# Kernel optimization log

Hardware: AMD Instinct MI355X
Metric: run time of the kernel (lower is better)

The kernel has to match this reference:

```python
import jax, jax.numpy as jnp
import numpy as np

N = 50000
E = 800000
IN_C, HID, OUT_C, HEADS = 128, 32, 64, 4
NEG_SLOPE = 0.2


def setup_inputs() -> dict:
    key = jax.random.key(0)
    ks = jax.random.split(key, 10)
    x = jax.random.normal(ks[0], (N, IN_C), dtype=jnp.float32)
    edge_index = jax.random.randint(ks[1], (2, E), 0, N, dtype=jnp.int64)
    s = 0.05
    W1 = jax.random.normal(ks[2], (IN_C, HID), dtype=jnp.float32) * s
    b1 = jnp.zeros((HID,), dtype=jnp.float32)
    Wg = jax.random.normal(ks[3], (HID, HEADS * HID), dtype=jnp.float32) * s
    ag_src = jax.random.normal(ks[4], (HEADS, HID), dtype=jnp.float32) * s
    ag_dst = jax.random.normal(ks[5], (HEADS, HID), dtype=jnp.float32) * s
    bg = jnp.zeros((HID,), dtype=jnp.float32)
    W2 = jax.random.normal(ks[6], (HID, OUT_C), dtype=jnp.float32) * s
    b2 = jnp.zeros((OUT_C,), dtype=jnp.float32)
    return {"x": x, "edge_index": edge_index, "W1": W1, "b1": b1,
            "Wg": Wg, "ag_src": ag_src, "ag_dst": ag_dst, "bg": bg,
            "W2": W2, "b2": b2}


def _add_self_loops(edge_index, n):
    loop = jnp.arange(n, dtype=edge_index.dtype)
    return jnp.concatenate([edge_index, jnp.stack([loop, loop])], axis=1)


def _gcn(x, src, dst, W, b, n):
    # PyG GCNConv: symmetric normalization with self-loops, scatter-add
    xw = x @ W  # [N, F]
    deg = jnp.zeros((n,), xw.dtype).at[dst].add(1.0)  # in-degree incl self-loops
    dinv = jax.lax.rsqrt(deg)
    norm = dinv[src] * dinv[dst]  # [E']
    msg = xw[src] * norm[:, None]  # [E', F]
    out = jax.ops.segment_sum(msg, dst, num_segments=n)
    return out + b


def _gat(x, src, dst, Wg, a_src, a_dst, b, n):
    # PyG GATConv, concat=False (mean over heads), leaky_relu slope 0.2
    h = (x @ Wg).reshape(n, HEADS, HID)  # [N, H, D]
    al_s = jnp.einsum('nhd,hd->nh', h, a_src)  # [N, H]
    al_d = jnp.einsum('nhd,hd->nh', h, a_dst)
    logits = jax.nn.leaky_relu(al_s[src] + al_d[dst], NEG_SLOPE)  # [E', H]
    # segment softmax over incoming edges of each dst node
    m = jax.ops.segment_max(logits, dst, num_segments=n)
    e = jnp.exp(logits - m[dst])
    denom = jax.ops.segment_sum(e, dst, num_segments=n)
    alpha = e / denom[dst]  # [E', H]
    msg = h[src] * alpha[:, :, None]  # [E', H, D]
    out = jax.ops.segment_sum(msg, dst, num_segments=n)  # [N, H, D]
    return out.mean(axis=1) + b


def reference(x, edge_index, W1, b1, Wg, ag_src, ag_dst, bg, W2, b2):
    ei = _add_self_loops(edge_index, N)
    src, dst = ei[0], ei[1]
    h = jax.nn.relu(_gcn(x, src, dst, W1, b1, N))
    h = jax.nn.relu(_gat(h, src, dst, Wg, ag_src, ag_dst, bg, N))
    return _gcn(h, src, dst, W2, b2, N)
```

## Files before the change

### kernel.cpp

```cpp
#include <hip/hip_runtime.h>
#include <hip/hip_bf16.h>

#define N_NODES 50000
#define N_EDGES 800000
#define EP (N_EDGES + N_NODES)
#define IN_C 128
#define HID 32
#define OUT_C 64
#define HEADS 4
#define NEG_SLOPE 0.2f

#define NPB 128
#define K_BUCKETS ((N_NODES + NPB - 1) / NPB)

typedef unsigned int uint32;

__device__ __forceinline__ float bf_lo(uint32 u) { return __uint_as_float(u << 16); }
__device__ __forceinline__ float bf_hi(uint32 u) { return __uint_as_float(u & 0xffff0000u); }
__device__ __forceinline__ uint32 f2bf(float f) {
    uint32 u = __float_as_uint(f);
    return (u + 0x7fffu + ((u >> 16) & 1u)) >> 16;
}
__device__ __forceinline__ uint32 pack_bf2(float a, float b) {
    return f2bf(a) | (f2bf(b) << 16);
}

__global__ __launch_bounds__(512) void k_init2(int* __restrict__ gcnt,
                                               const float* __restrict__ Wg,
                                               const float* __restrict__ ags,
                                               const float* __restrict__ agd,
                                               float* __restrict__ wals,
                                               float* __restrict__ wald,
                                               const float* __restrict__ W2,
                                               uint32* __restrict__ wgp,
                                               uint32* __restrict__ w2p) {
    int t = threadIdx.x;
    if (t < K_BUCKETS + 1) gcnt[t] = 0;
    if (t < 256) {
        int c = t & 127;
        int h = c >> 5, k = c & 31;
        const float* a = (t < 128) ? ags : agd;
        float acc = 0.f;
#pragma unroll
        for (int d = 0; d < 32; d++) acc += Wg[k * 128 + h * 32 + d] * a[h * 32 + d];
        if (t < 128) wals[c] = acc; else wald[c] = acc;
    }
    for (int i = t; i < 2048; i += 512) {
        int j4 = i >> 6, d = (i >> 1) & 31, pp = i & 1;
        int c0 = 4 * j4 + 2 * pp, c1 = c0 + 1;
        float a = Wg[(c0 & 31) * 128 + (c0 >> 5) * 32 + d];
        float b = Wg[(c1 & 31) * 128 + (c1 >> 5) * 32 + d];
        wgp[i] = pack_bf2(a, b);
    }
    for (int i = t; i < 1024; i += 512) {
        int k4 = i >> 7, d = (i >> 1) & 63, pp = i & 1;
        int r0 = 4 * k4 + 2 * pp, r1 = r0 + 1;
        w2p[i] = pack_bf2(W2[r0 * 64 + d], W2[r1 * 64 + d]);
    }
}


__global__ __launch_bounds__(256) void k_bcount(const int* __restrict__ ei,
                                                int* __restrict__ gcnt) {
    __shared__ int h[K_BUCKETS];
    int t = threadIdx.x;
    for (int i = t; i < K_BUCKETS; i += 256) h[i] = 0;
    __syncthreads();
    int base = blockIdx.x * 4096;
    int dd[16];
#pragma unroll
    for (int k = 0; k < 16; k++) {
        int e = base + k * 256 + t;
        dd[k] = (e < N_EDGES) ? ei[N_EDGES + e] : -1;
    }
#pragma unroll
    for (int k = 0; k < 16; k++)
        if (dd[k] >= 0) atomicAdd(&h[dd[k] >> 7], 1);
    __syncthreads();
    for (int i = t; i < K_BUCKETS; i += 256)
        if (h[i]) atomicAdd(&gcnt[i], h[i]);
}

__global__ __launch_bounds__(512) void k_bscan(const int* __restrict__ gcnt,
                                               int* __restrict__ gbase,
                                               int* __restrict__ gcursor) {
    __shared__ int sd[512];
    int t = threadIdx.x;
    int v = (t < K_BUCKETS) ? gcnt[t] : 0;
    sd[t] = v;
    __syncthreads();
    for (int off = 1; off < 512; off <<= 1) {
        int x = (t >= off) ? sd[t - off] : 0;
        __syncthreads();
        sd[t] += x;
        __syncthreads();
    }
    if (t < K_BUCKETS) {
        int excl = sd[t] - v;
        gbase[t] = excl;
        gcursor[t] = excl;
    }
    if (t == 0) gbase[K_BUCKETS] = sd[K_BUCKETS - 1];
}

__global__ __launch_bounds__(256) void k_bucket(const int* __restrict__ ei,
                                                int* __restrict__ gcursor,
                                                uint32* __restrict__ gpairs) {
    __shared__ int cnt[K_BUCKETS];
    __shared__ int bas[K_BUCKETS];
    int t = threadIdx.x;
    for (int i = t; i < K_BUCKETS; i += 256) cnt[i] = 0;
    __syncthreads();
    int base = blockIdx.x * 2048;
    int ss[8], dd[8], ml[8];
#pragma unroll
    for (int k = 0; k < 8; k++) {
        int e = base + k * 256 + t;
        ss[k] = (e < N_EDGES) ? ei[e] : -1;
        dd[k] = (e < N_EDGES) ? ei[N_EDGES + e] : 0;
    }
#pragma unroll
    for (int k = 0; k < 8; k++)
        if (ss[k] >= 0) ml[k] = atomicAdd(&cnt[dd[k] >> 7], 1);
    __syncthreads();
    for (int i = t; i < K_BUCKETS; i += 256)
        bas[i] = cnt[i] ? atomicAdd(&gcursor[i], cnt[i]) : 0;
    __syncthreads();
#pragma unroll
    for (int k = 0; k < 8; k++)
        if (ss[k] >= 0)
            gpairs[bas[dd[k] >> 7] + ml[k]] = ((uint32)ss[k] << 7) | (uint32)(dd[k] & 127);
}

__global__ __launch_bounds__(256) void k_node(const uint32* __restrict__ gpairs,
                                              const int* __restrict__ gbase,
                                              int* __restrict__ offs,
                                              float* __restrict__ dinv,
                                              int* __restrict__ srcs) {
    __shared__ int cnt[NPB];
    __shared__ int scn[NPB];
    __shared__ int cur[NPB];
    int t = threadIdx.x;
    int b = blockIdx.x;
    int lo = b << 7;
    int nn = N_NODES - lo; if (nn > NPB) nn = NPB;
    int pb = gbase[b], pe = gbase[b + 1];
    if (t < NPB) cnt[t] = 0;
    __syncthreads();
    for (int i = pb + t; i < pe; i += 256)
        atomicAdd(&cnt[gpairs[i] & 127], 1);
    __syncthreads();
    if (t < NPB) scn[t] = cnt[t];
    __syncthreads();
    for (int off = 1; off < NPB; off <<= 1) {
        int x = 0;
        if (t >= off && t < NPB) x = scn[t - off];
        __syncthreads();
        if (t < NPB) scn[t] += x;
        __syncthreads();
    }
    if (t < nn) {
        int excl = scn[t] - cnt[t];
        int o = pb + excl + lo + t;
        offs[lo + t] = o;
        cur[t] = o;
        dinv[lo + t] = rsqrtf((float)(cnt[t] + 1));
        srcs[pb + scn[t] + lo + t] = lo + t;
    }
    if (b == K_BUCKETS - 1 && t == 0) offs[N_NODES] = pe + N_NODES;
    __syncthreads();
    for (int i = pb + t; i < pe; i += 256) {
        uint32 u = gpairs[i];
        int pos = atomicAdd(&cur[u & 127], 1);
        srcs[pos] = (int)(u >> 7);
    }
}

__global__ __launch_bounds__(256) void k_gemm1(const float* __restrict__ x,
                                               const float* __restrict__ W1,
                                               const float* __restrict__ dinv,
                                               uint32* __restrict__ xw1) {
    __shared__ float wl[IN_C * HID];
    __shared__ float xl[8 * IN_C];
    int t = threadIdx.x;
    for (int i = t; i < IN_C * HID; i += 256) {
        int k = i >> 5, f = i & 31;
        wl[(k >> 1) * 64 + f * 2 + (k & 1)] = W1[i];
    }
    int nb = blockIdx.x * 8;
    const float4* x4 = (const float4*)(x + (size_t)nb * IN_C);
    ((float4*)xl)[t] = x4[t];
    __syncthreads();
    int g = t >> 5, f = t & 31;
    const float2* xr = (const float2*)(xl + g * IN_C);
    const float2* wp = (const float2*)wl;
    float acc = 0.f;
#pragma unroll 16
    for (int k2 = 0; k2 < 64; k2++) {
        float2 xv = xr[k2];
        float2 wv = wp[k2 * 32 + f];
        acc += xv.x * wv.x + xv.y * wv.y;
    }
    float v = acc * dinv[nb + g];
    float vn = __shfl_xor(v, 1, 64);
    if ((f & 1) == 0) xw1[(size_t)(nb + g) * 16 + (f >> 1)] = pack_bf2(v, vn);
}

__global__ __launch_bounds__(256) void k_gather1(const uint32* __restrict__ xw1,
                                                 const int* __restrict__ offs,
                                                 const int* __restrict__ srcs,
                                                 const float* __restrict__ dinv,
                                                 const float* __restrict__ b1,
                                                 const float* __restrict__ wals,
                                                 const float* __restrict__ wald,
                                                 uint32* __restrict__ h1s,
                                                 float* __restrict__ als,
                                                 float* __restrict__ ald) {
    int t = threadIdx.x;
    int l16 = t & 15;
    int n = blockIdx.x * 16 + (t >> 4);
    int s0 = offs[n], s1 = offs[n + 1];
    const uint32* xc = xw1 + l16;
    float a0 = 0.f, a1 = 0.f, a2 = 0.f, a3 = 0.f;
    int j = s0;
    for (; j + 1 < s1; j += 2) {
        uint32 uA = xc[(size_t)srcs[j] * 16];
        uint32 uB = xc[(size_t)srcs[j + 1] * 16];
        a0 += bf_lo(uA); a1 += bf_hi(uA);
        a2 += bf_lo(uB); a3 += bf_hi(uB);
    }
    if (j < s1) {
        uint32 uA = xc[(size_t)srcs[j] * 16];
        a0 += bf_lo(uA); a1 += bf_hi(uA);
    }
    float dn = dinv[n];
    float2 b = ((const float2*)b1)[l16];
    float vx = (a0 + a2) * dn + b.x;
    float vy = (a1 + a3) * dn + b.y;
    vx = vx > 0.f ? vx : 0.f;
    vy = vy > 0.f ? vy : 0.f;
    h1s[(size_t)n * 16 + l16] = pack_bf2(vx, vy);

    float ps0, ps1, ps2, ps3, pd0, pd1, pd2, pd3;
    {
        float2 w0 = ((const float2*)wals)[0 * 16 + l16];
        float2 w1 = ((const float2*)wals)[1 * 16 + l16];
        float2 w2 = ((const float2*)wals)[2 * 16 + l16];
        float2 w3 = ((const float2*)wals)[3 * 16 + l16];
        ps0 = vx * w0.x + vy * w0.y;
        ps1 = vx * w1.x + vy * w1.y;
        ps2 = vx * w2.x + vy * w2.y;
        ps3 = vx * w3.x + vy * w3.y;
        float2 u0 = ((const float2*)wald)[0 * 16 + l16];
        float2 u1 = ((const float2*)wald)[1 * 16 + l16];
        float2 u2 = ((const float2*)wald)[2 * 16 + l16];
        float2 u3 = ((const float2*)wald)[3 * 16 + l16];
        pd0 = vx * u0.x + vy * u0.y;
        pd1 = vx * u1.x + vy * u1.y;
        pd2 = vx * u2.x + vy * u2.y;
        pd3 = vx * u3.x + vy * u3.y;
    }
#pragma unroll
    for (int m = 1; m < 16; m <<= 1) {
        ps0 += __shfl_xor(ps0, m, 16); ps1 += __shfl_xor(ps1, m, 16);
        ps2 += __shfl_xor(ps2, m, 16); ps3 += __shfl_xor(ps3, m, 16);
        pd0 += __shfl_xor(pd0, m, 16); pd1 += __shfl_xor(pd1, m, 16);
        pd2 += __shfl_xor(pd2, m, 16); pd3 += __shfl_xor(pd3, m, 16);
    }
    if (l16 == 0) {
        als[n * 4 + 0] = ps0; als[n * 4 + 1] = ps1;
        als[n * 4 + 2] = ps2; als[n * 4 + 3] = ps3;
        ald[n * 4 + 0] = pd0; ald[n * 4 + 1] = pd1;
        ald[n * 4 + 2] = pd2; ald[n * 4 + 3] = pd3;
    }
}

__global__ __launch_bounds__(256) void k_gat_agg(const uint32* __restrict__ h1s,
                                                 const float* __restrict__ als,
                                                 const float* __restrict__ ald,
                                                 const int* __restrict__ offs,
                                                 const int* __restrict__ srcs,
                                                 const uint32* __restrict__ wgp,
                                                 const float* __restrict__ bg,
                                                 const float* __restrict__ dinv,
                                                 uint32* __restrict__ h2s) {
    __shared__ __align__(16) uint32 wl[2048];
    __shared__ __align__(16) uint32 gl[8][64];
    int t = threadIdx.x;
    {
        const uint4* src4 = (const uint4*)wgp;
        uint4* dst4 = (uint4*)wl;
        dst4[t] = src4[t];
        dst4[256 + t] = src4[256 + t];
    }

    int l32 = t & 31;
    int hb = t & 32;
    int g8 = t >> 5;
    int n = blockIdx.x * 8 + g8;
    int h = l32 >> 3, e8 = l32 & 7;
    int l16 = l32 & 15;
    int h16 = (l32 >> 4) & 1;
    int s0 = offs[n], s1 = offs[n + 1];
    float ad = ald[n * 4 + h];
    const uint32* rowp = h1s + l16;

    float g00 = 0.f, g01 = 0.f, g10 = 0.f, g11 = 0.f;
    float g20 = 0.f, g21 = 0.f, g30 = 0.f, g31 = 0.f;
    float ssum = 0.f;
    for (int base = s0; base < s1; base += 8) {
        int jj = base + e8;
        int sA = 0; float wt = 0.f;
        if (jj < s1) {
            sA = srcs[jj];
            float l = als[sA * 4 + h] + ad;
            l = l > 0.f ? l : NEG_SLOPE * l;
            wt = __expf(l);
        }
        ssum += wt;
        int cnt = s1 - base; if (cnt > 8) cnt = 8;
#pragma unroll
        for (int q = 0; q < 8; q += 2) {
            int eq = q + h16;
            int   sq = __shfl(sA, hb + eq, 64);
            float w0 = __shfl(wt, hb + eq, 64);
            float w1 = __shfl(wt, hb + 8 + eq, 64);
            float w2 = __shfl(wt, hb + 16 + eq, 64);
            float w3 = __shfl(wt, hb + 24 + eq, 64);
            if (eq < cnt) {
                uint32 u = rowp[(size_t)sq * 16];
                float flo = bf_lo(u), fhi = bf_hi(u);
                g00 += w0 * flo; g01 += w0 * fhi;
                g10 += w1 * flo; g11 += w1 * fhi;
                g20 += w2 * flo; g21 += w2 * fhi;
                g30 += w3 * flo; g31 += w3 * fhi;
            }
        }
    }
    ssum += __shfl_xor(ssum, 1, 64);
    ssum += __shfl_xor(ssum, 2, 64);
    ssum += __shfl_xor(ssum, 4, 64);
    float inv = 0.25f / ssum;
    float inv0 = __shfl(inv, hb + 0, 64);
    float inv1 = __shfl(inv, hb + 8, 64);
    float inv2 = __shfl(inv, hb + 16, 64);
    float inv3 = __shfl(inv, hb + 24, 64);
    g00 += __shfl_xor(g00, 16, 64); g01 += __shfl_xor(g01, 16, 64);
    g10 += __shfl_xor(g10, 16, 64); g11 += __shfl_xor(g11, 16, 64);
    g20 += __shfl_xor(g20, 16, 64); g21 += __shfl_xor(g21, 16, 64);
    g30 += __shfl_xor(g30, 16, 64); g31 += __shfl_xor(g31, 16, 64);
    if (l32 < 16) {
        gl[g8][0 * 16 + l16] = pack_bf2(g00 * inv0, g01 * inv0);
        gl[g8][1 * 16 + l16] = pack_bf2(g10 * inv1, g11 * inv1);
        gl[g8][2 * 16 + l16] = pack_bf2(g20 * inv2, g21 * inv2);
        gl[g8][3 * 16 + l16] = pack_bf2(g30 * inv3, g31 * inv3);
    }
    __syncthreads();
    const uint2* gv = (const uint2*)gl[g8];
    const uint2* wp = (const uint2*)wl;
    int d = l32;
    float acc = 0.f;
#pragma unroll 8
    for (int j4 = 0; j4 < 32; j4++) {
        uint2 gg = gv[j4];
        uint2 ww = wp[j4 * 32 + d];
        acc += bf_lo(gg.x) * bf_lo(ww.x) + bf_hi(gg.x) * bf_hi(ww.x)
             + bf_lo(gg.y) * bf_lo(ww.y) + bf_hi(gg.y) * bf_hi(ww.y);
    }
    float v = acc + bg[d];
    v = v > 0.f ? v : 0.f;
    v *= dinv[n];
    float vn = __shfl_xor(v, 1, 64);
    if ((d & 1) == 0) h2s[(size_t)n * 16 + (d >> 1)] = pack_bf2(v, vn);
}

__global__ __launch_bounds__(256) void k_gather2(const uint32* __restrict__ h2s,
                                                 const int* __restrict__ offs,
                                                 const int* __restrict__ srcs,
                                                 const uint32* __restrict__ w2p,
                                                 const float* __restrict__ dinv,
                                                 const float* __restrict__ b2,
                                                 float* __restrict__ out) {
    __shared__ __align__(16) uint32 wl[1024];
    __shared__ __align__(16) uint32 gbf[16][16];
    int t = threadIdx.x;
    ((uint4*)wl)[t] = ((const uint4*)w2p)[t];

    int l16 = t & 15;
    int g16 = t >> 4;
    int n = blockIdx.x * 16 + g16;
    int s0 = offs[n], s1 = offs[n + 1];
    const uint32* xc = h2s + l16;
    float a0 = 0.f, a1 = 0.f, a2 = 0.f, a3 = 0.f;
    int j = s0;
    for (; j + 1 < s1; j += 2) {
        uint32 uA = xc[(size_t)srcs[j] * 16];
        uint32 uB = xc[(size_t)srcs[j + 1] * 16];
        a0 += bf_lo(uA); a1 += bf_hi(uA);
        a2 += bf_lo(uB); a3 += bf_hi(uB);
    }
    if (j < s1) {
        uint32 uA = xc[(size_t)srcs[j] * 16];
        a0 += bf_lo(uA); a1 += bf_hi(uA);
    }
    gbf[g16][l16] = pack_bf2(a0 + a2, a1 + a3);
    __syncthreads();
    const uint2* gv = (const uint2*)gbf[g16];
    const uint2* wp = (const uint2*)wl;
    float dn = dinv[n];
    float acc0 = 0.f, acc1 = 0.f, acc2 = 0.f, acc3 = 0.f;
#pragma unroll
    for (int k4 = 0; k4 < 8; k4++) {
        uint2 gg = gv[k4];
        float gx = bf_lo(gg.x), gy = bf_hi(gg.x);
        float gz = bf_lo(gg.y), gw = bf_hi(gg.y);
        uint2 w0 = wp[k4 * 64 + l16];
        uint2 w1 = wp[k4 * 64 + l16 + 16];
        uint2 w2 = wp[k4 * 64 + l16 + 32];
        uint2 w3 = wp[k4 * 64 + l16 + 48];
        acc0 += gx * bf_lo(w0.x) + gy * bf_hi(w0.x) + gz * bf_lo(w0.y) + gw * bf_hi(w0.y);
        acc1 += gx * bf_lo(w1.x) + gy * bf_hi(w1.x) + gz * bf_lo(w1.y) + gw * bf_hi(w1.y);
        acc2 += gx * bf_lo(w2.x) + gy * bf_hi(w2.x) + gz * bf_lo(w2.y) + gw * bf_hi(w2.y);
        acc3 += gx * bf_lo(w3.x) + gy * bf_hi(w3.x) + gz * bf_lo(w3.y) + gw * bf_hi(w3.y);
    }
    float* op = out + (size_t)n * OUT_C;
    op[l16]      = acc0 * dn + b2[l16];
    op[l16 + 16] = acc1 * dn + b2[l16 + 16];
    op[l16 + 32] = acc2 * dn + b2[l16 + 32];
    op[l16 + 48] = acc3 * dn + b2[l16 + 48];
}

extern "C" void kernel_launch(void* const* d_in, const int* in_sizes, int n_in,
                              void* d_out, int out_size, void* d_ws, size_t ws_size,
                              hipStream_t stream) {
    const float* x   = (const float*)d_in[0];
    const int*   ei  = (const int*)d_in[1];
    const float* W1  = (const float*)d_in[2];
    const float* b1  = (const float*)d_in[3];
    const float* Wg  = (const float*)d_in[4];
    const float* ags = (const float*)d_in[5];
    const float* agd = (const float*)d_in[6];
    const float* bg  = (const float*)d_in[7];
    const float* W2  = (const float*)d_in[8];
    const float* b2  = (const float*)d_in[9];
    float* out = (float*)d_out;

    char* p = (char*)d_ws;
    auto alloc = [&](size_t bytes) -> void* {
        void* r = (void*)p;
        p += (bytes + 255) & ~(size_t)255;
        return r;
    };
    float*  dinv    = (float*)alloc((size_t)N_NODES * 4);
    int*    offs    = (int*)  alloc((size_t)(N_NODES + 1) * 4);
    int*    gcnt    = (int*)  alloc((size_t)(K_BUCKETS + 1) * 4);
    int*    gbase   = (int*)  alloc((size_t)(K_BUCKETS + 1) * 4);
    int*    gcursor = (int*)  alloc((size_t)(K_BUCKETS + 1) * 4);
    int*    srcs    = (int*)  alloc((size_t)EP * 4);
    uint32* gpairs  = (uint32*)alloc((size_t)N_EDGES * 4);
    uint32* xw1     = (uint32*)alloc((size_t)N_NODES * 16 * 4);
    uint32* h1s     = (uint32*)alloc((size_t)N_NODES * 16 * 4);
    float*  als     = (float*)alloc((size_t)N_NODES * HEADS * 4);
    float*  ald     = (float*)alloc((size_t)N_NODES * HEADS * 4);
    float*  wals    = (float*)alloc(128 * 4);
    float*  wald    = (float*)alloc(128 * 4);
    uint32* wgp     = (uint32*)alloc(2048 * 4);
    uint32* w2p     = (uint32*)alloc(1024 * 4);
    uint32* h2s     = (uint32*)alloc((size_t)N_NODES * 16 * 4);

    k_init2<<<1, 512, 0, stream>>>(gcnt, Wg, ags, agd, wals, wald, W2, wgp, w2p);
    k_bcount<<<(N_EDGES + 4095) / 4096, 256, 0, stream>>>(ei, gcnt);
    k_bscan<<<1, 512, 0, stream>>>(gcnt, gbase, gcursor);
    k_bucket<<<(N_EDGES + 2047) / 2048, 256, 0, stream>>>(ei, gcursor, gpairs);
    k_node<<<K_BUCKETS, 256, 0, stream>>>(gpairs, gbase, offs, dinv, srcs);

    k_gemm1<<<N_NODES / 8, 256, 0, stream>>>(x, W1, dinv, xw1);
    k_gather1<<<N_NODES / 16, 256, 0, stream>>>(xw1, offs, srcs, dinv, b1,
                                                wals, wald, h1s, als, ald);

    k_gat_agg<<<N_NODES / 8, 256, 0, stream>>>(h1s, als, ald, offs, srcs,
                                               wgp, bg, dinv, h2s);

    k_gather2<<<N_NODES / 16, 256, 0, stream>>>(h2s, offs, srcs, w2p, dinv, b2, out);
}
```

Measured before the change: 236.9 us.

## Precompute per-node exponentials so GAT edge weights need only multiplies

The GAT attention weight exp(leaky_relu(as+ad)) is factored into per-node exponentials exp(as), exp(0.2*as), exp(ad), exp(0.2*ad), computed once in the gather1 kernel. Each edge weight becomes a product, and the branch is chosen by testing whether the product exceeds 1, so no per-edge exp is needed. The aggregation loop is also restructured: each half-wave handles alternate edges directly and keeps per-head sums, removing the shuffle-based broadcast of weights and indices. Per-node storage doubles, and the softmax skips max subtraction as before, so exponentials of large logits could overflow.

```diff
diff --git a/kernel.cpp b/kernel.cpp
--- a/kernel.cpp
+++ b/kernel.cpp
@@ -214,8 +214,8 @@
                                                  const float* __restrict__ wals,
                                                  const float* __restrict__ wald,
                                                  uint32* __restrict__ h1s,
-                                                 float* __restrict__ als,
-                                                 float* __restrict__ ald) {
+                                                 float* __restrict__ eals,
+                                                 float* __restrict__ eald) {
     int t = threadIdx.x;
     int l16 = t & 15;
     int n = blockIdx.x * 16 + (t >> 4);
@@ -268,16 +268,20 @@
         pd2 += __shfl_xor(pd2, m, 16); pd3 += __shfl_xor(pd3, m, 16);
     }
     if (l16 == 0) {
-        als[n * 4 + 0] = ps0; als[n * 4 + 1] = ps1;
-        als[n * 4 + 2] = ps2; als[n * 4 + 3] = ps3;
-        ald[n * 4 + 0] = pd0; ald[n * 4 + 1] = pd1;
-        ald[n * 4 + 2] = pd2; ald[n * 4 + 3] = pd3;
+        float4* es = (float4*)(eals + (size_t)n * 8);
+        float4* ed = (float4*)(eald + (size_t)n * 8);
+        es[0] = make_float4(__expf(ps0), __expf(ps1), __expf(ps2), __expf(ps3));
+        es[1] = make_float4(__expf(NEG_SLOPE * ps0), __expf(NEG_SLOPE * ps1),
+                            __expf(NEG_SLOPE * ps2), __expf(NEG_SLOPE * ps3));
+        ed[0] = make_float4(__expf(pd0), __expf(pd1), __expf(pd2), __expf(pd3));
+        ed[1] = make_float4(__expf(NEG_SLOPE * pd0), __expf(NEG_SLOPE * pd1),
+                            __expf(NEG_SLOPE * pd2), __expf(NEG_SLOPE * pd3));
     }
 }
 
 __global__ __launch_bounds__(256) void k_gat_agg(const uint32* __restrict__ h1s,
-                                                 const float* __restrict__ als,
-                                                 const float* __restrict__ ald,
+                                                 const float* __restrict__ eals,
+                                                 const float* __restrict__ eald,
                                                  const int* __restrict__ offs,
                                                  const int* __restrict__ srcs,
                                                  const uint32* __restrict__ wgp,
@@ -295,65 +299,58 @@
     }
 
     int l32 = t & 31;
-    int hb = t & 32;
     int g8 = t >> 5;
     int n = blockIdx.x * 8 + g8;
-    int h = l32 >> 3, e8 = l32 & 7;
     int l16 = l32 & 15;
-    int h16 = (l32 >> 4) & 1;
+    int par = l32 >> 4;
     int s0 = offs[n], s1 = offs[n + 1];
-    float ad = ald[n * 4 + h];
-    const uint32* rowp = h1s + l16;
+    const float4* edp = (const float4*)(eald + (size_t)n * 8);
+    float4 d1 = edp[0];
+    float4 d2 = edp[1];
 
     float g00 = 0.f, g01 = 0.f, g10 = 0.f, g11 = 0.f;
     float g20 = 0.f, g21 = 0.f, g30 = 0.f, g31 = 0.f;
-    float ssum = 0.f;
-    for (int base = s0; base < s1; base += 8) {
-        int jj = base + e8;
-        int sA = 0; float wt = 0.f;
-        if (jj < s1) {
-            sA = srcs[jj];
-            float l = als[sA * 4 + h] + ad;
-            l = l > 0.f ? l : NEG_SLOPE * l;
-            wt = __expf(l);
-        }
-        ssum += wt;
-        int cnt = s1 - base; if (cnt > 8) cnt = 8;
-#pragma unroll
-        for (int q = 0; q < 8; q += 2) {
-            int eq = q + h16;
-            int   sq = __shfl(sA, hb + eq, 64);
-            float w0 = __shfl(wt, hb + eq, 64);
-            float w1 = __shfl(wt, hb + 8 + eq, 64);
-            float w2 = __shfl(wt, hb + 16 + eq, 64);
-            float w3 = __shfl(wt, hb + 24 + eq, 64);
-            if (eq < cnt) {
-                uint32 u = rowp[(size_t)sq * 16];
-                float flo = bf_lo(u), fhi = bf_hi(u);
-                g00 += w0 * flo; g01 += w0 * fhi;
-                g10 += w1 * flo; g11 += w1 * fhi;
-                g20 += w2 * flo; g21 += w2 * fhi;
-                g30 += w3 * flo; g31 += w3 * fhi;
-            }
-        }
-    }
-    ssum += __shfl_xor(ssum, 1, 64);
-    ssum += __shfl_xor(ssum, 2, 64);
-    ssum += __shfl_xor(ssum, 4, 64);
-    float inv = 0.25f / ssum;
-    float inv0 = __shfl(inv, hb + 0, 64);
-    float inv1 = __shfl(inv, hb + 8, 64);
-    float inv2 = __shfl(inv, hb + 16, 64);
-    float inv3 = __shfl(inv, hb + 24, 64);
+    float ss0 = 0.f, ss1 = 0.f, ss2 = 0.f, ss3 = 0.f;
+
+#define GAT_EDGE(J)                                                            \
+    {                                                                          \
+        int sq = srcs[J];                                                      \
+        const float4* esp = (const float4*)(eals + (size_t)sq * 8);            \
+        float4 e1 = esp[0];                                                    \
+        float4 e2 = esp[1];                                                    \
+        uint32 u = h1s[(size_t)sq * 16 + l16];                                 \
+        float flo = bf_lo(u), fhi = bf_hi(u);                                  \
+        float p, q, w;                                                         \
+        p = e1.x * d1.x; q = e2.x * d2.x; w = p > 1.f ? p : q;                 \
+        ss0 += w; g00 += w * flo; g01 += w * fhi;                              \
+        p = e1.y * d1.y; q = e2.y * d2.y; w = p > 1.f ? p : q;                 \
+        ss1 += w; g10 += w * flo; g11 += w * fhi;                              \
+        p = e1.z * d1.z; q = e2.z * d2.z; w = p > 1.f ? p : q;                 \
+        ss2 += w; g20 += w * flo; g21 += w * fhi;                              \
+        p = e1.w * d1.w; q = e2.w * d2.w; w = p > 1.f ? p : q;                 \
+        ss3 += w; g30 += w * flo; g31 += w * fhi;                              \
+    }
+
+    int j = s0 + par;
+    for (; j + 2 < s1; j += 4) {
+        GAT_EDGE(j);
+        GAT_EDGE(j + 2);
+    }
+    if (j < s1) GAT_EDGE(j);
+#undef GAT_EDGE
+
+    ss0 += __shfl_xor(ss0, 16, 64); ss1 += __shfl_xor(ss1, 16, 64);
+    ss2 += __shfl_xor(ss2, 16, 64); ss3 += __shfl_xor(ss3, 16, 64);
     g00 += __shfl_xor(g00, 16, 64); g01 += __shfl_xor(g01, 16, 64);
     g10 += __shfl_xor(g10, 16, 64); g11 += __shfl_xor(g11, 16, 64);
     g20 += __shfl_xor(g20, 16, 64); g21 += __shfl_xor(g21, 16, 64);
     g30 += __shfl_xor(g30, 16, 64); g31 += __shfl_xor(g31, 16, 64);
+    float i0 = 0.25f / ss0, i1 = 0.25f / ss1, i2 = 0.25f / ss2, i3 = 0.25f / ss3;
     if (l32 < 16) {
-        gl[g8][0 * 16 + l16] = pack_bf2(g00 * inv0, g01 * inv0);
-        gl[g8][1 * 16 + l16] = pack_bf2(g10 * inv1, g11 * inv1);
-        gl[g8][2 * 16 + l16] = pack_bf2(g20 * inv2, g21 * inv2);
-        gl[g8][3 * 16 + l16] = pack_bf2(g30 * inv3, g31 * inv3);
+        gl[g8][0 * 16 + l16] = pack_bf2(g00 * i0, g01 * i0);
+        gl[g8][1 * 16 + l16] = pack_bf2(g10 * i1, g11 * i1);
+        gl[g8][2 * 16 + l16] = pack_bf2(g20 * i2, g21 * i2);
+        gl[g8][3 * 16 + l16] = pack_bf2(g30 * i3, g31 * i3);
     }
     __syncthreads();
     const uint2* gv = (const uint2*)gl[g8];
@@ -460,8 +457,8 @@
     uint32* gpairs  = (uint32*)alloc((size_t)N_EDGES * 4);
     uint32* xw1     = (uint32*)alloc((size_t)N_NODES * 16 * 4);
     uint32* h1s     = (uint32*)alloc((size_t)N_NODES * 16 * 4);
-    float*  als     = (float*)alloc((size_t)N_NODES * HEADS * 4);
-    float*  ald     = (float*)alloc((size_t)N_NODES * HEADS * 4);
+    float*  eals    = (float*)alloc((size_t)N_NODES * 8 * 4);
+    float*  eald    = (float*)alloc((size_t)N_NODES * 8 * 4);
     float*  wals    = (float*)alloc(128 * 4);
     float*  wald    = (float*)alloc(128 * 4);
     uint32* wgp     = (uint32*)alloc(2048 * 4);
@@ -476,9 +473,9 @@
 
     k_gemm1<<<N_NODES / 8, 256, 0, stream>>>(x, W1, dinv, xw1);
     k_gather1<<<N_NODES / 16, 256, 0, stream>>>(xw1, offs, srcs, dinv, b1,
-                                                wals, wald, h1s, als, ald);
-
-    k_gat_agg<<<N_NODES / 8, 256, 0, stream>>>(h1s, als, ald, offs, srcs,
+                                                wals, wald, h1s, eals, eald);
+
+    k_gat_agg<<<N_NODES / 8, 256, 0, stream>>>(h1s, eals, eald, offs, srcs,
                                                wgp, bg, dinv, h2s);
 
     k_gather2<<<N_NODES / 16, 256, 0, stream>>>(h2s, offs, srcs, w2p, dinv, b2, out);
```

After: 236.2 us. No clear change (-0.3%).
